# Optimization experiments

Hardware: AMD Instinct MI355X
Metric: run time of the kernel (lower is better)

Reference implementation:

```python
import jax, jax.numpy as jnp
import numpy as np

LR = 0.1
N_HEADS = 4


def setup_inputs() -> dict:
    key = jax.random.key(0)
    ks = jax.random.split(key, 12)
    B, S, D, M, H = 2, 1024, 128, 512, 512
    s = 0.05
    return {
        "x": jax.random.normal(ks[0], (B, S, D), jnp.float32),
        "memory": jax.random.normal(ks[1], (M, D), jnp.float32) * s,
        "w_q": jax.random.normal(ks[2], (D, D), jnp.float32) * s,
        "w_k": jax.random.normal(ks[3], (D, D), jnp.float32) * s,
        "w_v": jax.random.normal(ks[4], (D, D), jnp.float32) * s,
        "b_q": jax.random.normal(ks[5], (D,), jnp.float32) * s,
        "b_k": jax.random.normal(ks[6], (D,), jnp.float32) * s,
        "b_v": jax.random.normal(ks[7], (D,), jnp.float32) * s,
        "w_o": jax.random.normal(ks[8], (D, D), jnp.float32) * s,
        "b_o": jax.random.normal(ks[9], (D,), jnp.float32) * s,
        "w_fc": jax.random.normal(ks[10], (H, D), jnp.float32) * s,
        "b_fc": jax.random.normal(ks[11], (H,), jnp.float32) * s,
    }


def reference(x, memory, w_q, w_k, w_v, b_q, b_k, b_v, w_o, b_o, w_fc, b_fc):
    B, S, D = x.shape
    M = memory.shape[0]
    hd = D // N_HEADS

    # --- LongTermMemory update (broadcast pairwise diff [B,S,M,D]) ---
    diff = x[:, :, None, :] - memory[None, None, :, :]          # [B,S,M,D]
    surprise = jnp.sqrt(jnp.sum(diff * diff, axis=-1, keepdims=True))  # [B,S,M,1]
    agg = jnp.mean(LR * surprise * diff, axis=(0, 1))           # [M,D]
    # torch does memory.data += agg (detached in-place update)
    mem = memory + jax.lax.stop_gradient(agg)                    # [M,D]

    # --- MultiheadAttention(query=x, key=mem, value=mem), batch_first ---
    # mem is identical across batch, so project once.
    q = (x @ w_q.T + b_q).reshape(B, S, N_HEADS, hd)
    k = (mem @ w_k.T + b_k).reshape(M, N_HEADS, hd)
    v = (mem @ w_v.T + b_v).reshape(M, N_HEADS, hd)
    scores = jnp.einsum('bshd,mhd->bhsm', q, k) / jnp.sqrt(jnp.asarray(hd, x.dtype))
    attn = jax.nn.softmax(scores, axis=-1)
    ctx = jnp.einsum('bhsm,mhd->bshd', attn, v).reshape(B, S, D)
    attn_out = ctx @ w_o.T + b_o                                 # [B,S,D]

    # --- Linear + ReLU ---
    return jax.nn.relu(attn_out @ w_fc.T + b_fc)                 # [B,S,hidden]
```

## Files before the change

kernel.cpp:

```cpp
#include <hip/hip_runtime.h>
#include <hip/hip_bf16.h>
#include <math.h>

#define SS 1024
#define MM 512
#define LRC (0.1f/2048.0f)
#define SCALE 0.17677669529663687f

typedef __attribute__((ext_vector_type(8))) short s8v;
typedef __attribute__((ext_vector_type(4))) float f32x4;
#define MFMA16(a, b, c) __builtin_amdgcn_mfma_f32_16x16x32_bf16(a, b, c, 0, 0, 0)

__device__ __forceinline__ unsigned short f2b(float f) {
  union { float f; unsigned int u; } v; v.f = f;
  return (unsigned short)((v.u + 0x7FFFu + ((v.u >> 16) & 1u)) >> 16);
}

__global__ __launch_bounds__(256) void k_p1(
    const float* __restrict__ x, const float* __restrict__ mem,
    const float* __restrict__ wq, const float* __restrict__ wk,
    const float* __restrict__ wv, const float* __restrict__ wo,
    const float* __restrict__ wfc, const float* __restrict__ bq,
    unsigned short* __restrict__ STb, unsigned short* __restrict__ xT,
    unsigned short* __restrict__ qbf,
    unsigned short* __restrict__ wkb, unsigned short* __restrict__ wvb,
    unsigned short* __restrict__ wob, unsigned short* __restrict__ wfcb) {
  __shared__ alignas(16) char smem[69376];
  const int t = threadIdx.x, bx = blockIdx.x;
  const int w = t >> 6, l = t & 63;
  const int kq = (l >> 4) * 8;
  const int r0l = (l >> 4) * 4;

  if (bx < 256) {
    float (*xl)[132]          = reinterpret_cast<float (*)[132]>(smem);
    unsigned short (*xb)[136] = reinterpret_cast<unsigned short (*)[136]>(smem + 33792);
    unsigned short (*mb)[136] = reinterpret_cast<unsigned short (*)[136]>(smem + 51200);
    float* xn                 = reinterpret_cast<float*>(smem + 68608);
    float* mn                 = reinterpret_cast<float*>(smem + 68864);
    const int bs0 = (bx & 31) * 64, m0 = (bx >> 5) * 64;

    for (int i = t; i < 2048; i += 256) {
      int r = i >> 5, c4 = (i & 31) * 4;
      float4 v = *reinterpret_cast<const float4*>(&x[(bs0 + r) * 128 + c4]);
      xl[r][c4] = v.x; xl[r][c4+1] = v.y; xl[r][c4+2] = v.z; xl[r][c4+3] = v.w;
      ushort4 u; u.x = f2b(v.x); u.y = f2b(v.y); u.z = f2b(v.z); u.w = f2b(v.w);
      *reinterpret_cast<ushort4*>(&xb[r][c4]) = u;
    }
    __syncthreads();
    {
      int r = t >> 2, q = t & 3;
      float s = 0.f;
      #pragma unroll
      for (int j = 0; j < 32; ++j) { float v = xl[r][q * 32 + j]; s += v * v; }
      s += __shfl_xor(s, 1); s += __shfl_xor(s, 2);
      if (q == 0) xn[r] = s;
    }
    if ((bx >> 5) == 0) {
      int d = t >> 1, hh = t & 1;
      #pragma unroll
      for (int j4 = 0; j4 < 32; j4 += 4) {
        ushort4 u;
        u.x = xb[hh*32 + j4    ][d];
        u.y = xb[hh*32 + j4 + 1][d];
        u.z = xb[hh*32 + j4 + 2][d];
        u.w = xb[hh*32 + j4 + 3][d];
        *reinterpret_cast<ushort4*>(&xT[d * 2048 + bs0 + hh*32 + j4]) = u;
      }
    }
    __syncthreads();
    for (int i = t; i < 2048; i += 256) {
      int r = i >> 5, c4 = (i & 31) * 4;
      float4 v = *reinterpret_cast<const float4*>(&mem[(m0 + r) * 128 + c4]);
      xl[r][c4] = v.x; xl[r][c4+1] = v.y; xl[r][c4+2] = v.z; xl[r][c4+3] = v.w;
      ushort4 u; u.x = f2b(v.x); u.y = f2b(v.y); u.z = f2b(v.z); u.w = f2b(v.w);
      *reinterpret_cast<ushort4*>(&mb[r][c4]) = u;
    }
    __syncthreads();
    {
      int r = t >> 2, q = t & 3;
      float s = 0.f;
      #pragma unroll
      for (int j = 0; j < 32; ++j) { float v = xl[r][q * 32 + j]; s += v * v; }
      s += __shfl_xor(s, 1); s += __shfl_xor(s, 2);
      if (q == 0) mn[r] = s;
    }
    __syncthreads();
    f32x4 acc[4] = {};
    #pragma unroll
    for (int kc = 0; kc < 4; ++kc) {
      s8v a = *reinterpret_cast<const s8v*>(&xb[w*16 + (l&15)][kc*32 + kq]);
      #pragma unroll
      for (int mt = 0; mt < 4; ++mt) {
        s8v b = *reinterpret_cast<const s8v*>(&mb[mt*16 + (l&15)][kc*32 + kq]);
        acc[mt] = MFMA16(a, b, acc[mt]);
      }
    }
    const int r0g = bs0 + w * 16 + r0l;
    float xnr[4];
    #pragma unroll
    for (int i = 0; i < 4; ++i) xnr[i] = xn[w*16 + r0l + i];
    #pragma unroll
    for (int mt = 0; mt < 4; ++mt) {
      const int coll = mt * 16 + (l & 15);
      const float mnv = mn[coll];
      ushort4 u;
      u.x = f2b(sqrtf(fmaxf(0.f, xnr[0] + mnv - 2.f * acc[mt][0])));
      u.y = f2b(sqrtf(fmaxf(0.f, xnr[1] + mnv - 2.f * acc[mt][1])));
      u.z = f2b(sqrtf(fmaxf(0.f, xnr[2] + mnv - 2.f * acc[mt][2])));
      u.w = f2b(sqrtf(fmaxf(0.f, xnr[3] + mnv - 2.f * acc[mt][3])));
      *reinterpret_cast<ushort4*>(&STb[(m0 + coll) * 2048 + r0g]) = u;
    }
  } else if (bx < 288) {
    unsigned short (*xb)[136]  = reinterpret_cast<unsigned short (*)[136]>(smem);
    unsigned short (*wql)[136] = reinterpret_cast<unsigned short (*)[136]>(smem + 17408);
    const int s0 = (bx - 256) * 64;
    for (int i = t; i < 2048; i += 256) {
      int r = i >> 5, c4 = (i & 31) * 4;
      float4 v = *reinterpret_cast<const float4*>(&x[(s0 + r) * 128 + c4]);
      ushort4 u; u.x = f2b(v.x); u.y = f2b(v.y); u.z = f2b(v.z); u.w = f2b(v.w);
      *reinterpret_cast<ushort4*>(&xb[r][c4]) = u;
    }
    for (int i = t; i < 4096; i += 256) {
      int r = i >> 5, c4 = (i & 31) * 4;
      float4 v = *reinterpret_cast<const float4*>(&wq[r * 128 + c4]);
      ushort4 u; u.x = f2b(v.x); u.y = f2b(v.y); u.z = f2b(v.z); u.w = f2b(v.w);
      *reinterpret_cast<ushort4*>(&wql[r][c4]) = u;
    }
    __syncthreads();
    f32x4 acc[8] = {};
    #pragma unroll
    for (int kc = 0; kc < 4; ++kc) {
      s8v a = *reinterpret_cast<const s8v*>(&xb[w*16 + (l&15)][kc*32 + kq]);
      #pragma unroll
      for (int nt = 0; nt < 8; ++nt) {
        s8v b = *reinterpret_cast<const s8v*>(&wql[nt*16 + (l&15)][kc*32 + kq]);
        acc[nt] = MFMA16(a, b, acc[nt]);
      }
    }
    const int r0g = s0 + w * 16 + r0l;
    #pragma unroll
    for (int nt = 0; nt < 8; ++nt) {
      const int col = nt * 16 + (l & 15);
      const float bb = bq[col];
      #pragma unroll
      for (int i = 0; i < 4; ++i)
        qbf[(r0g + i) * 128 + col] = f2b((acc[nt][i] + bb) * SCALE);
    }
  } else {
    const float* src; unsigned short* dst; int off = 0;
    if (bx == 288)      { src = wk;  dst = wkb; }
    else if (bx == 289) { src = wv;  dst = wvb; }
    else if (bx == 290) { src = wo;  dst = wob; }
    else                { src = wfc; dst = wfcb; off = (bx - 291) * 16384; }
    for (int i = t; i < 4096; i += 256) {
      float4 v = *reinterpret_cast<const float4*>(&src[off + i * 4]);
      ushort4 u; u.x = f2b(v.x); u.y = f2b(v.y); u.z = f2b(v.z); u.w = f2b(v.w);
      *reinterpret_cast<ushort4*>(&dst[off + i * 4]) = u;
    }
  }
}

__global__ __launch_bounds__(256) void k_p2(
    const unsigned short* __restrict__ STb, const unsigned short* __restrict__ xT,
    const float* __restrict__ mem,
    const unsigned short* __restrict__ wkb, const unsigned short* __restrict__ wvb,
    const float* __restrict__ bk, const float* __restrict__ bv,
    unsigned short* __restrict__ kbf, unsigned short* __restrict__ vT) {
  __shared__ float Tld[16][132];
  __shared__ float srowl[16];
  __shared__ unsigned short mnl[16][136];
  const int t = threadIdx.x;
  const int w = t >> 6, l = t & 63;
  const int kq = (l >> 4) * 8;
  const int r0l = (l >> 4) * 4;
  const int m0 = blockIdx.x * 16;

  f32x4 acc[2] = {};
  float ssum = 0.f;
  const int arow = m0 + (l & 15);
  #pragma unroll 4
  for (int kk = 0; kk < 64; ++kk) {
    s8v a = *reinterpret_cast<const s8v*>(&STb[arow * 2048 + kk * 32 + kq]);
    #pragma unroll
    for (int j = 0; j < 8; ++j) {
      union { unsigned int u; float f; } cv;
      cv.u = ((unsigned int)(unsigned short)a[j]) << 16;
      ssum += cv.f;
    }
    #pragma unroll
    for (int nt = 0; nt < 2; ++nt) {
      s8v b = *reinterpret_cast<const s8v*>(&xT[(w*32 + nt*16 + (l&15)) * 2048 + kk*32 + kq]);
      acc[nt] = MFMA16(a, b, acc[nt]);
    }
  }
  ssum += __shfl_xor(ssum, 16); ssum += __shfl_xor(ssum, 32);
  if (w == 0 && l < 16) srowl[l] = ssum;
  #pragma unroll
  for (int nt = 0; nt < 2; ++nt) {
    const int col = w * 32 + nt * 16 + (l & 15);
    #pragma unroll
    for (int i = 0; i < 4; ++i) Tld[r0l + i][col] = acc[nt][i];
  }
  __syncthreads();
  #pragma unroll
  for (int i = 0; i < 8; ++i) {
    const int flat = t + 256 * i;
    const int r = flat >> 7, c = flat & 127;
    const float mv = mem[(m0 + r) * 128 + c];
    mnl[r][c] = f2b(mv + LRC * (Tld[r][c] - srowl[r] * mv));
  }
  __syncthreads();
  #pragma unroll
  for (int p = 0; p < 2; ++p) {
    const unsigned short* W = p ? wvb : wkb;
    const float* bias = p ? bv : bk;
    f32x4 pacc[2] = {};
    #pragma unroll
    for (int kc = 0; kc < 4; ++kc) {
      s8v a = *reinterpret_cast<const s8v*>(&mnl[l & 15][kc * 32 + kq]);
      #pragma unroll
      for (int nt = 0; nt < 2; ++nt) {
        s8v b = *reinterpret_cast<const s8v*>(&W[(w*32 + nt*16 + (l&15)) * 128 + kc*32 + kq]);
        pacc[nt] = MFMA16(a, b, pacc[nt]);
      }
    }
    #pragma unroll
    for (int nt = 0; nt < 2; ++nt) {
      const int col = w * 32 + nt * 16 + (l & 15);
      const float bb = bias[col];
      if (p == 0) {
        #pragma unroll
        for (int i = 0; i < 4; ++i)
          kbf[(m0 + r0l + i) * 128 + col] = f2b(pacc[nt][i] + bb);
      } else {
        ushort4 u;
        u.x = f2b(pacc[nt][0] + bb); u.y = f2b(pacc[nt][1] + bb);
        u.z = f2b(pacc[nt][2] + bb); u.w = f2b(pacc[nt][3] + bb);
        *reinterpret_cast<ushort4*>(&vT[col * 512 + m0 + r0l]) = u;
      }
    }
  }
}

__global__ __launch_bounds__(256) void k_p3(
    const unsigned short* __restrict__ qbf, const unsigned short* __restrict__ kbf,
    const unsigned short* __restrict__ vT, const unsigned short* __restrict__ wob,
    const unsigned short* __restrict__ wfcb, const float* __restrict__ bo,
    const float* __restrict__ bfc, float* __restrict__ out) {
  __shared__ alignas(16) char smem[75264];
  unsigned short (*Pl)[520] = reinterpret_cast<unsigned short (*)[520]>(smem);
  unsigned short (*cl)[136] = reinterpret_cast<unsigned short (*)[136]>(smem + 66560);
  unsigned short (*al)[136] = reinterpret_cast<unsigned short (*)[136]>(smem + 70912);
  const int t = threadIdx.x;
  const int w = t >> 6, l = t & 63;
  const int kq = (l >> 4) * 8;
  const int r0l = (l >> 4) * 4;
  const int r0 = blockIdx.x * 16;

  {
    const int h = w;
    const s8v a = *reinterpret_cast<const s8v*>(&qbf[(r0 + (l & 15)) * 128 + h * 32 + kq]);
    f32x4 acc[32];
    #pragma unroll
    for (int mt = 0; mt < 32; ++mt) acc[mt] = f32x4{0.f, 0.f, 0.f, 0.f};
    #pragma unroll
    for (int mt = 0; mt < 32; ++mt) {
      s8v b2 = *reinterpret_cast<const s8v*>(&kbf[(mt*16 + (l&15)) * 128 + h*32 + kq]);
      acc[mt] = MFMA16(a, b2, acc[mt]);
    }
    #pragma unroll
    for (int i = 0; i < 4; ++i) {
      float mx = acc[0][i];
      #pragma unroll
      for (int mt = 1; mt < 32; ++mt) mx = fmaxf(mx, acc[mt][i]);
      mx = fmaxf(mx, __shfl_xor(mx, 1));
      mx = fmaxf(mx, __shfl_xor(mx, 2));
      mx = fmaxf(mx, __shfl_xor(mx, 4));
      mx = fmaxf(mx, __shfl_xor(mx, 8));
      float sm = 0.f;
      #pragma unroll
      for (int mt = 0; mt < 32; ++mt) {
        float e = __expf(acc[mt][i] - mx); acc[mt][i] = e; sm += e;
      }
      sm += __shfl_xor(sm, 1); sm += __shfl_xor(sm, 2);
      sm += __shfl_xor(sm, 4); sm += __shfl_xor(sm, 8);
      const float inv = 1.f / sm;
      #pragma unroll
      for (int mt = 0; mt < 32; ++mt)
        Pl[h * 16 + r0l + i][mt * 16 + (l & 15)] = f2b(acc[mt][i] * inv);
    }
  }
  __syncthreads();
  {
    const int h = w;
    f32x4 acc[2] = {};
    #pragma unroll 4
    for (int kk = 0; kk < 16; ++kk) {
      s8v a = *reinterpret_cast<const s8v*>(&Pl[h * 16 + (l & 15)][kk * 32 + kq]);
      #pragma unroll
      for (int nt = 0; nt < 2; ++nt) {
        s8v b2 = *reinterpret_cast<const s8v*>(&vT[(h*32 + nt*16 + (l&15)) * 512 + kk*32 + kq]);
        acc[nt] = MFMA16(a, b2, acc[nt]);
      }
    }
    #pragma unroll
    for (int nt = 0; nt < 2; ++nt) {
      const int col = h * 32 + nt * 16 + (l & 15);
      #pragma unroll
      for (int i = 0; i < 4; ++i) cl[r0l + i][col] = f2b(acc[nt][i]);
    }
  }
  __syncthreads();
  {
    f32x4 acc[2] = {};
    #pragma unroll
    for (int kc = 0; kc < 4; ++kc) {
      s8v a = *reinterpret_cast<const s8v*>(&cl[l & 15][kc * 32 + kq]);
      #pragma unroll
      for (int nt = 0; nt < 2; ++nt) {
        s8v b2 = *reinterpret_cast<const s8v*>(&wob[(w*32 + nt*16 + (l&15)) * 128 + kc*32 + kq]);
        acc[nt] = MFMA16(a, b2, acc[nt]);
      }
    }
    #pragma unroll
    for (int nt = 0; nt < 2; ++nt) {
      const int col = w * 32 + nt * 16 + (l & 15);
      const float bb = bo[col];
      #pragma unroll
      for (int i = 0; i < 4; ++i) al[r0l + i][col] = f2b(acc[nt][i] + bb);
    }
  }
  __syncthreads();
  {
    f32x4 acc[8] = {};
    #pragma unroll
    for (int kc = 0; kc < 4; ++kc) {
      s8v a = *reinterpret_cast<const s8v*>(&al[l & 15][kc * 32 + kq]);
      #pragma unroll
      for (int nt = 0; nt < 8; ++nt) {
        s8v b2 = *reinterpret_cast<const s8v*>(&wfcb[(w*128 + nt*16 + (l&15)) * 128 + kc*32 + kq]);
        acc[nt] = MFMA16(a, b2, acc[nt]);
      }
    }
    #pragma unroll
    for (int nt = 0; nt < 8; ++nt) {
      const int col = w * 128 + nt * 16 + (l & 15);
      const float bb = bfc[col];
      #pragma unroll
      for (int i = 0; i < 4; ++i)
        out[(r0 + r0l + i) * 512 + col] = fmaxf(acc[nt][i] + bb, 0.f);
    }
  }
}

extern "C" void kernel_launch(void* const* d_in, const int* in_sizes, int n_in,
                              void* d_out, int out_size, void* d_ws, size_t ws_size,
                              hipStream_t stream) {
  const float* x    = (const float*)d_in[0];
  const float* mem  = (const float*)d_in[1];
  const float* w_q  = (const float*)d_in[2];
  const float* w_k  = (const float*)d_in[3];
  const float* w_v  = (const float*)d_in[4];
  const float* b_q  = (const float*)d_in[5];
  const float* b_k  = (const float*)d_in[6];
  const float* b_v  = (const float*)d_in[7];
  const float* w_o  = (const float*)d_in[8];
  const float* b_o  = (const float*)d_in[9];
  const float* w_fc = (const float*)d_in[10];
  const float* b_fc = (const float*)d_in[11];
  float* out = (float*)d_out;

  char* base = (char*)d_ws;
  unsigned short* STb  = (unsigned short*)(base);
  unsigned short* xT   = (unsigned short*)(base + 2097152);
  unsigned short* qbf  = (unsigned short*)(base + 2621440);
  unsigned short* kbf  = (unsigned short*)(base + 3145728);
  unsigned short* vT   = (unsigned short*)(base + 3276800);
  unsigned short* wkb  = (unsigned short*)(base + 3407872);
  unsigned short* wvb  = (unsigned short*)(base + 3440640);
  unsigned short* wob  = (unsigned short*)(base + 3473408);
  unsigned short* wfcb = (unsigned short*)(base + 3506176);

  k_p1<<<295, 256, 0, stream>>>(x, mem, w_q, w_k, w_v, w_o, w_fc, b_q,
                                STb, xT, qbf, wkb, wvb, wob, wfcb);
  k_p2<<<32, 256, 0, stream>>>(STb, xT, mem, wkb, wvb, b_k, b_v, kbf, vT);
  k_p3<<<128, 256, 0, stream>>>(qbf, kbf, vT, wob, wfcb, b_o, b_fc, out);
}
```

Measured before the change: 58.91 us.

## Move Q projection and weight casts into second kernel, slim first kernel

The first kernel now handles only the pairwise-distance tiles. It computes row norms from registers with wave shuffles instead of staging fp32 data in LDS, which lowers shared-memory use and removes barriers. The Q projection and the wo/wfc casts move into the second kernel, running alongside its 32 memory-update blocks so that the mostly idle second launch gets more parallel work. The memory-update blocks now cast wk/wv to bf16 themselves into LDS, so each of the 32 blocks repeats that conversion.

```diff
diff --git a/kernel.cpp b/kernel.cpp
--- a/kernel.cpp
+++ b/kernel.cpp
@@ -18,226 +18,258 @@
 
 __global__ __launch_bounds__(256) void k_p1(
     const float* __restrict__ x, const float* __restrict__ mem,
-    const float* __restrict__ wq, const float* __restrict__ wk,
-    const float* __restrict__ wv, const float* __restrict__ wo,
-    const float* __restrict__ wfc, const float* __restrict__ bq,
-    unsigned short* __restrict__ STb, unsigned short* __restrict__ xT,
-    unsigned short* __restrict__ qbf,
-    unsigned short* __restrict__ wkb, unsigned short* __restrict__ wvb,
-    unsigned short* __restrict__ wob, unsigned short* __restrict__ wfcb) {
-  __shared__ alignas(16) char smem[69376];
+    unsigned short* __restrict__ STb, unsigned short* __restrict__ xT) {
+  __shared__ unsigned short xb[64][136];
+  __shared__ unsigned short mb[64][136];
+  __shared__ float xn[64];
+  __shared__ float mn[64];
   const int t = threadIdx.x, bx = blockIdx.x;
   const int w = t >> 6, l = t & 63;
   const int kq = (l >> 4) * 8;
   const int r0l = (l >> 4) * 4;
-
-  if (bx < 256) {
-    float (*xl)[132]          = reinterpret_cast<float (*)[132]>(smem);
-    unsigned short (*xb)[136] = reinterpret_cast<unsigned short (*)[136]>(smem + 33792);
-    unsigned short (*mb)[136] = reinterpret_cast<unsigned short (*)[136]>(smem + 51200);
-    float* xn                 = reinterpret_cast<float*>(smem + 68608);
-    float* mn                 = reinterpret_cast<float*>(smem + 68864);
-    const int bs0 = (bx & 31) * 64, m0 = (bx >> 5) * 64;
-
-    for (int i = t; i < 2048; i += 256) {
-      int r = i >> 5, c4 = (i & 31) * 4;
-      float4 v = *reinterpret_cast<const float4*>(&x[(bs0 + r) * 128 + c4]);
-      xl[r][c4] = v.x; xl[r][c4+1] = v.y; xl[r][c4+2] = v.z; xl[r][c4+3] = v.w;
+  const int bs0 = (bx & 31) * 64, m0 = (bx >> 5) * 64;
+  const int rB = t >> 5;
+  const int c4 = (t & 31) * 4;
+
+  {
+    float p[8];
+    #pragma unroll
+    for (int k = 0; k < 8; ++k) {
+      const int r = rB + 8 * k;
+      const float4 v = *reinterpret_cast<const float4*>(&x[(bs0 + r) * 128 + c4]);
+      p[k] = v.x*v.x + v.y*v.y + v.z*v.z + v.w*v.w;
       ushort4 u; u.x = f2b(v.x); u.y = f2b(v.y); u.z = f2b(v.z); u.w = f2b(v.w);
       *reinterpret_cast<ushort4*>(&xb[r][c4]) = u;
     }
-    __syncthreads();
-    {
-      int r = t >> 2, q = t & 3;
-      float s = 0.f;
-      #pragma unroll
-      for (int j = 0; j < 32; ++j) { float v = xl[r][q * 32 + j]; s += v * v; }
-      s += __shfl_xor(s, 1); s += __shfl_xor(s, 2);
-      if (q == 0) xn[r] = s;
-    }
-    if ((bx >> 5) == 0) {
-      int d = t >> 1, hh = t & 1;
-      #pragma unroll
-      for (int j4 = 0; j4 < 32; j4 += 4) {
-        ushort4 u;
-        u.x = xb[hh*32 + j4    ][d];
-        u.y = xb[hh*32 + j4 + 1][d];
-        u.z = xb[hh*32 + j4 + 2][d];
-        u.w = xb[hh*32 + j4 + 3][d];
-        *reinterpret_cast<ushort4*>(&xT[d * 2048 + bs0 + hh*32 + j4]) = u;
-      }
-    }
-    __syncthreads();
-    for (int i = t; i < 2048; i += 256) {
-      int r = i >> 5, c4 = (i & 31) * 4;
-      float4 v = *reinterpret_cast<const float4*>(&mem[(m0 + r) * 128 + c4]);
-      xl[r][c4] = v.x; xl[r][c4+1] = v.y; xl[r][c4+2] = v.z; xl[r][c4+3] = v.w;
+    #pragma unroll
+    for (int k = 0; k < 8; ++k) {
+      float s = p[k];
+      s += __shfl_xor(s, 1);  s += __shfl_xor(s, 2);
+      s += __shfl_xor(s, 4);  s += __shfl_xor(s, 8);
+      s += __shfl_xor(s, 16);
+      if ((t & 31) == 0) xn[rB + 8 * k] = s;
+    }
+  }
+  {
+    float p[8];
+    #pragma unroll
+    for (int k = 0; k < 8; ++k) {
+      const int r = rB + 8 * k;
+      const float4 v = *reinterpret_cast<const float4*>(&mem[(m0 + r) * 128 + c4]);
+      p[k] = v.x*v.x + v.y*v.y + v.z*v.z + v.w*v.w;
       ushort4 u; u.x = f2b(v.x); u.y = f2b(v.y); u.z = f2b(v.z); u.w = f2b(v.w);
       *reinterpret_cast<ushort4*>(&mb[r][c4]) = u;
     }
-    __syncthreads();
-    {
-      int r = t >> 2, q = t & 3;
-      float s = 0.f;
-      #pragma unroll
-      for (int j = 0; j < 32; ++j) { float v = xl[r][q * 32 + j]; s += v * v; }
-      s += __shfl_xor(s, 1); s += __shfl_xor(s, 2);
-      if (q == 0) mn[r] = s;
-    }
-    __syncthreads();
-    f32x4 acc[4] = {};
-    #pragma unroll
-    for (int kc = 0; kc < 4; ++kc) {
-      s8v a = *reinterpret_cast<const s8v*>(&xb[w*16 + (l&15)][kc*32 + kq]);
-      #pragma unroll
-      for (int mt = 0; mt < 4; ++mt) {
-        s8v b = *reinterpret_cast<const s8v*>(&mb[mt*16 + (l&15)][kc*32 + kq]);
-        acc[mt] = MFMA16(a, b, acc[mt]);
-      }
-    }
-    const int r0g = bs0 + w * 16 + r0l;
-    float xnr[4];
-    #pragma unroll
-    for (int i = 0; i < 4; ++i) xnr[i] = xn[w*16 + r0l + i];
+    #pragma unroll
+    for (int k = 0; k < 8; ++k) {
+      float s = p[k];
+      s += __shfl_xor(s, 1);  s += __shfl_xor(s, 2);
+      s += __shfl_xor(s, 4);  s += __shfl_xor(s, 8);
+      s += __shfl_xor(s, 16);
+      if ((t & 31) == 0) mn[rB + 8 * k] = s;
+    }
+  }
+  __syncthreads();
+
+  if ((bx >> 5) == 0) {
+    int d = t >> 1, hh = t & 1;
+    #pragma unroll
+    for (int j4 = 0; j4 < 32; j4 += 4) {
+      ushort4 u;
+      u.x = xb[hh*32 + j4    ][d];
+      u.y = xb[hh*32 + j4 + 1][d];
+      u.z = xb[hh*32 + j4 + 2][d];
+      u.w = xb[hh*32 + j4 + 3][d];
+      *reinterpret_cast<ushort4*>(&xT[d * 2048 + bs0 + hh*32 + j4]) = u;
+    }
+  }
+
+  f32x4 acc[4] = {};
+  #pragma unroll
+  for (int kc = 0; kc < 4; ++kc) {
+    s8v a = *reinterpret_cast<const s8v*>(&xb[w*16 + (l&15)][kc*32 + kq]);
     #pragma unroll
     for (int mt = 0; mt < 4; ++mt) {
-      const int coll = mt * 16 + (l & 15);
-      const float mnv = mn[coll];
-      ushort4 u;
-      u.x = f2b(sqrtf(fmaxf(0.f, xnr[0] + mnv - 2.f * acc[mt][0])));
-      u.y = f2b(sqrtf(fmaxf(0.f, xnr[1] + mnv - 2.f * acc[mt][1])));
-      u.z = f2b(sqrtf(fmaxf(0.f, xnr[2] + mnv - 2.f * acc[mt][2])));
-      u.w = f2b(sqrtf(fmaxf(0.f, xnr[3] + mnv - 2.f * acc[mt][3])));
-      *reinterpret_cast<ushort4*>(&STb[(m0 + coll) * 2048 + r0g]) = u;
-    }
-  } else if (bx < 288) {
-    unsigned short (*xb)[136]  = reinterpret_cast<unsigned short (*)[136]>(smem);
-    unsigned short (*wql)[136] = reinterpret_cast<unsigned short (*)[136]>(smem + 17408);
-    const int s0 = (bx - 256) * 64;
-    for (int i = t; i < 2048; i += 256) {
-      int r = i >> 5, c4 = (i & 31) * 4;
-      float4 v = *reinterpret_cast<const float4*>(&x[(s0 + r) * 128 + c4]);
-      ushort4 u; u.x = f2b(v.x); u.y = f2b(v.y); u.z = f2b(v.z); u.w = f2b(v.w);
-      *reinterpret_cast<ushort4*>(&xb[r][c4]) = u;
-    }
-    for (int i = t; i < 4096; i += 256) {
-      int r = i >> 5, c4 = (i & 31) * 4;
-      float4 v = *reinterpret_cast<const float4*>(&wq[r * 128 + c4]);
-      ushort4 u; u.x = f2b(v.x); u.y = f2b(v.y); u.z = f2b(v.z); u.w = f2b(v.w);
-      *reinterpret_cast<ushort4*>(&wql[r][c4]) = u;
-    }
-    __syncthreads();
-    f32x4 acc[8] = {};
-    #pragma unroll
-    for (int kc = 0; kc < 4; ++kc) {
-      s8v a = *reinterpret_cast<const s8v*>(&xb[w*16 + (l&15)][kc*32 + kq]);
-      #pragma unroll
-      for (int nt = 0; nt < 8; ++nt) {
-        s8v b = *reinterpret_cast<const s8v*>(&wql[nt*16 + (l&15)][kc*32 + kq]);
-        acc[nt] = MFMA16(a, b, acc[nt]);
-      }
-    }
-    const int r0g = s0 + w * 16 + r0l;
-    #pragma unroll
-    for (int nt = 0; nt < 8; ++nt) {
-      const int col = nt * 16 + (l & 15);
-      const float bb = bq[col];
-      #pragma unroll
-      for (int i = 0; i < 4; ++i)
-        qbf[(r0g + i) * 128 + col] = f2b((acc[nt][i] + bb) * SCALE);
-    }
-  } else {
-    const float* src; unsigned short* dst; int off = 0;
-    if (bx == 288)      { src = wk;  dst = wkb; }
-    else if (bx == 289) { src = wv;  dst = wvb; }
-    else if (bx == 290) { src = wo;  dst = wob; }
-    else                { src = wfc; dst = wfcb; off = (bx - 291) * 16384; }
-    for (int i = t; i < 4096; i += 256) {
-      float4 v = *reinterpret_cast<const float4*>(&src[off + i * 4]);
-      ushort4 u; u.x = f2b(v.x); u.y = f2b(v.y); u.z = f2b(v.z); u.w = f2b(v.w);
-      *reinterpret_cast<ushort4*>(&dst[off + i * 4]) = u;
-    }
+      s8v b = *reinterpret_cast<const s8v*>(&mb[mt*16 + (l&15)][kc*32 + kq]);
+      acc[mt] = MFMA16(a, b, acc[mt]);
+    }
+  }
+  const int r0g = bs0 + w * 16 + r0l;
+  float xnr[4];
+  #pragma unroll
+  for (int i = 0; i < 4; ++i) xnr[i] = xn[w*16 + r0l + i];
+  #pragma unroll
+  for (int mt = 0; mt < 4; ++mt) {
+    const int coll = mt * 16 + (l & 15);
+    const float mnv = mn[coll];
+    ushort4 u;
+    u.x = f2b(sqrtf(fmaxf(0.f, xnr[0] + mnv - 2.f * acc[mt][0])));
+    u.y = f2b(sqrtf(fmaxf(0.f, xnr[1] + mnv - 2.f * acc[mt][1])));
+    u.z = f2b(sqrtf(fmaxf(0.f, xnr[2] + mnv - 2.f * acc[mt][2])));
+    u.w = f2b(sqrtf(fmaxf(0.f, xnr[3] + mnv - 2.f * acc[mt][3])));
+    *reinterpret_cast<ushort4*>(&STb[(m0 + coll) * 2048 + r0g]) = u;
   }
 }
 
 __global__ __launch_bounds__(256) void k_p2(
     const unsigned short* __restrict__ STb, const unsigned short* __restrict__ xT,
-    const float* __restrict__ mem,
-    const unsigned short* __restrict__ wkb, const unsigned short* __restrict__ wvb,
-    const float* __restrict__ bk, const float* __restrict__ bv,
-    unsigned short* __restrict__ kbf, unsigned short* __restrict__ vT) {
-  __shared__ float Tld[16][132];
-  __shared__ float srowl[16];
-  __shared__ unsigned short mnl[16][136];
-  const int t = threadIdx.x;
+    const float* __restrict__ x, const float* __restrict__ mem,
+    const float* __restrict__ wq, const float* __restrict__ wk,
+    const float* __restrict__ wv, const float* __restrict__ wo,
+    const float* __restrict__ wfc,
+    const float* __restrict__ bq, const float* __restrict__ bk,
+    const float* __restrict__ bv,
+    unsigned short* __restrict__ qbf, unsigned short* __restrict__ kbf,
+    unsigned short* __restrict__ vT,
+    unsigned short* __restrict__ wob, unsigned short* __restrict__ wfcb) {
+  __shared__ alignas(16) char smem[52224];
+  const int t = threadIdx.x, bx = blockIdx.x;
   const int w = t >> 6, l = t & 63;
   const int kq = (l >> 4) * 8;
   const int r0l = (l >> 4) * 4;
-  const int m0 = blockIdx.x * 16;
-
-  f32x4 acc[2] = {};
-  float ssum = 0.f;
-  const int arow = m0 + (l & 15);
-  #pragma unroll 4
-  for (int kk = 0; kk < 64; ++kk) {
-    s8v a = *reinterpret_cast<const s8v*>(&STb[arow * 2048 + kk * 32 + kq]);
-    #pragma unroll
-    for (int j = 0; j < 8; ++j) {
-      union { unsigned int u; float f; } cv;
-      cv.u = ((unsigned int)(unsigned short)a[j]) << 16;
-      ssum += cv.f;
-    }
-    #pragma unroll
-    for (int nt = 0; nt < 2; ++nt) {
-      s8v b = *reinterpret_cast<const s8v*>(&xT[(w*32 + nt*16 + (l&15)) * 2048 + kk*32 + kq]);
-      acc[nt] = MFMA16(a, b, acc[nt]);
-    }
-  }
-  ssum += __shfl_xor(ssum, 16); ssum += __shfl_xor(ssum, 32);
-  if (w == 0 && l < 16) srowl[l] = ssum;
-  #pragma unroll
-  for (int nt = 0; nt < 2; ++nt) {
-    const int col = w * 32 + nt * 16 + (l & 15);
-    #pragma unroll
-    for (int i = 0; i < 4; ++i) Tld[r0l + i][col] = acc[nt][i];
-  }
-  __syncthreads();
-  #pragma unroll
-  for (int i = 0; i < 8; ++i) {
-    const int flat = t + 256 * i;
-    const int r = flat >> 7, c = flat & 127;
-    const float mv = mem[(m0 + r) * 128 + c];
-    mnl[r][c] = f2b(mv + LRC * (Tld[r][c] - srowl[r] * mv));
-  }
-  __syncthreads();
-  #pragma unroll
-  for (int p = 0; p < 2; ++p) {
-    const unsigned short* W = p ? wvb : wkb;
-    const float* bias = p ? bv : bk;
-    f32x4 pacc[2] = {};
-    #pragma unroll
-    for (int kc = 0; kc < 4; ++kc) {
-      s8v a = *reinterpret_cast<const s8v*>(&mnl[l & 15][kc * 32 + kq]);
+
+  if (bx < 32) {
+    float (*Tld)[132]          = reinterpret_cast<float (*)[132]>(smem);
+    float* srowl               = reinterpret_cast<float*>(smem + 8448);
+    unsigned short (*mnl)[136] = reinterpret_cast<unsigned short (*)[136]>(smem + 8512);
+    unsigned short (*wl)[136]  = reinterpret_cast<unsigned short (*)[136]>(smem + 12864);
+    const int m0 = bx * 16;
+
+    f32x4 acc[2] = {};
+    float ssum = 0.f;
+    const int arow = m0 + (l & 15);
+    #pragma unroll 4
+    for (int kk = 0; kk < 64; ++kk) {
+      s8v a = *reinterpret_cast<const s8v*>(&STb[arow * 2048 + kk * 32 + kq]);
+      #pragma unroll
+      for (int j = 0; j < 8; ++j) {
+        union { unsigned int u; float f; } cv;
+        cv.u = ((unsigned int)(unsigned short)a[j]) << 16;
+        ssum += cv.f;
+      }
       #pragma unroll
       for (int nt = 0; nt < 2; ++nt) {
-        s8v b = *reinterpret_cast<const s8v*>(&W[(w*32 + nt*16 + (l&15)) * 128 + kc*32 + kq]);
-        pacc[nt] = MFMA16(a, b, pacc[nt]);
-      }
-    }
+        s8v b = *reinterpret_cast<const s8v*>(&xT[(w*32 + nt*16 + (l&15)) * 2048 + kk*32 + kq]);
+        acc[nt] = MFMA16(a, b, acc[nt]);
+      }
+    }
+    ssum += __shfl_xor(ssum, 16); ssum += __shfl_xor(ssum, 32);
+    if (w == 0 && l < 16) srowl[l] = ssum;
     #pragma unroll
     for (int nt = 0; nt < 2; ++nt) {
       const int col = w * 32 + nt * 16 + (l & 15);
-      const float bb = bias[col];
-      if (p == 0) {
+      #pragma unroll
+      for (int i = 0; i < 4; ++i) Tld[r0l + i][col] = acc[nt][i];
+    }
+    __syncthreads();
+    #pragma unroll
+    for (int i = 0; i < 8; ++i) {
+      const int flat = t + 256 * i;
+      const int r = flat >> 7, c = flat & 127;
+      const float mv = mem[(m0 + r) * 128 + c];
+      mnl[r][c] = f2b(mv + LRC * (Tld[r][c] - srowl[r] * mv));
+    }
+    __syncthreads();
+    for (int i = t; i < 4096; i += 256) {
+      int r = i >> 5, c4 = (i & 31) * 4;
+      float4 v = *reinterpret_cast<const float4*>(&wk[r * 128 + c4]);
+      ushort4 u; u.x = f2b(v.x); u.y = f2b(v.y); u.z = f2b(v.z); u.w = f2b(v.w);
+      *reinterpret_cast<ushort4*>(&wl[r][c4]) = u;
+    }
+    __syncthreads();
+    {
+      f32x4 pacc[2] = {};
+      #pragma unroll
+      for (int kc = 0; kc < 4; ++kc) {
+        s8v a = *reinterpret_cast<const s8v*>(&mnl[l & 15][kc * 32 + kq]);
+        #pragma unroll
+        for (int nt = 0; nt < 2; ++nt) {
+          s8v b = *reinterpret_cast<const s8v*>(&wl[(w*32 + nt*16 + (l&15))][kc*32 + kq]);
+          pacc[nt] = MFMA16(a, b, pacc[nt]);
+        }
+      }
+      #pragma unroll
+      for (int nt = 0; nt < 2; ++nt) {
+        const int col = w * 32 + nt * 16 + (l & 15);
+        const float bb = bk[col];
         #pragma unroll
         for (int i = 0; i < 4; ++i)
           kbf[(m0 + r0l + i) * 128 + col] = f2b(pacc[nt][i] + bb);
-      } else {
+      }
+    }
+    __syncthreads();
+    for (int i = t; i < 4096; i += 256) {
+      int r = i >> 5, c4 = (i & 31) * 4;
+      float4 v = *reinterpret_cast<const float4*>(&wv[r * 128 + c4]);
+      ushort4 u; u.x = f2b(v.x); u.y = f2b(v.y); u.z = f2b(v.z); u.w = f2b(v.w);
+      *reinterpret_cast<ushort4*>(&wl[r][c4]) = u;
+    }
+    __syncthreads();
+    {
+      f32x4 pacc[2] = {};
+      #pragma unroll
+      for (int kc = 0; kc < 4; ++kc) {
+        s8v a = *reinterpret_cast<const s8v*>(&mnl[l & 15][kc * 32 + kq]);
+        #pragma unroll
+        for (int nt = 0; nt < 2; ++nt) {
+          s8v b = *reinterpret_cast<const s8v*>(&wl[(w*32 + nt*16 + (l&15))][kc*32 + kq]);
+          pacc[nt] = MFMA16(a, b, pacc[nt]);
+        }
+      }
+      #pragma unroll
+      for (int nt = 0; nt < 2; ++nt) {
+        const int col = w * 32 + nt * 16 + (l & 15);
+        const float bb = bv[col];
         ushort4 u;
         u.x = f2b(pacc[nt][0] + bb); u.y = f2b(pacc[nt][1] + bb);
         u.z = f2b(pacc[nt][2] + bb); u.w = f2b(pacc[nt][3] + bb);
         *reinterpret_cast<ushort4*>(&vT[col * 512 + m0 + r0l]) = u;
       }
+    }
+  } else if (bx < 64) {
+    unsigned short (*xb)[136]  = reinterpret_cast<unsigned short (*)[136]>(smem);
+    unsigned short (*wql)[136] = reinterpret_cast<unsigned short (*)[136]>(smem + 17408);
+    const int s0 = (bx - 32) * 64;
+    for (int i = t; i < 2048; i += 256) {
+      int r = i >> 5, c4 = (i & 31) * 4;
+      float4 v = *reinterpret_cast<const float4*>(&x[(s0 + r) * 128 + c4]);
+      ushort4 u; u.x = f2b(v.x); u.y = f2b(v.y); u.z = f2b(v.z); u.w = f2b(v.w);
+      *reinterpret_cast<ushort4*>(&xb[r][c4]) = u;
+    }
+    for (int i = t; i < 4096; i += 256) {
+      int r = i >> 5, c4 = (i & 31) * 4;
+      float4 v = *reinterpret_cast<const float4*>(&wq[r * 128 + c4]);
+      ushort4 u; u.x = f2b(v.x); u.y = f2b(v.y); u.z = f2b(v.z); u.w = f2b(v.w);
+      *reinterpret_cast<ushort4*>(&wql[r][c4]) = u;
+    }
+    __syncthreads();
+    f32x4 acc[8] = {};
+    #pragma unroll
+    for (int kc = 0; kc < 4; ++kc) {
+      s8v a = *reinterpret_cast<const s8v*>(&xb[w*16 + (l&15)][kc*32 + kq]);
+      #pragma unroll
+      for (int nt = 0; nt < 8; ++nt) {
+        s8v b = *reinterpret_cast<const s8v*>(&wql[nt*16 + (l&15)][kc*32 + kq]);
+        acc[nt] = MFMA16(a, b, acc[nt]);
+      }
+    }
+    const int r0g = s0 + w * 16 + r0l;
+    #pragma unroll
+    for (int nt = 0; nt < 8; ++nt) {
+      const int col = nt * 16 + (l & 15);
+      const float bb = bq[col];
+      #pragma unroll
+      for (int i = 0; i < 4; ++i)
+        qbf[(r0g + i) * 128 + col] = f2b((acc[nt][i] + bb) * SCALE);
+    }
+  } else {
+    const float* src; unsigned short* dst; int off = 0;
+    if (bx == 64) { src = wo;  dst = wob; }
+    else          { src = wfc; dst = wfcb; off = (bx - 65) * 16384; }
+    for (int i = t; i < 4096; i += 256) {
+      float4 v = *reinterpret_cast<const float4*>(&src[off + i * 4]);
+      ushort4 u; u.x = f2b(v.x); u.y = f2b(v.y); u.z = f2b(v.z); u.w = f2b(v.w);
+      *reinterpret_cast<ushort4*>(&dst[off + i * 4]) = u;
     }
   }
 }
@@ -376,13 +408,11 @@
   unsigned short* qbf  = (unsigned short*)(base + 2621440);
   unsigned short* kbf  = (unsigned short*)(base + 3145728);
   unsigned short* vT   = (unsigned short*)(base + 3276800);
-  unsigned short* wkb  = (unsigned short*)(base + 3407872);
-  unsigned short* wvb  = (unsigned short*)(base + 3440640);
-  unsigned short* wob  = (unsigned short*)(base + 3473408);
-  unsigned short* wfcb = (unsigned short*)(base + 3506176);
-
-  k_p1<<<295, 256, 0, stream>>>(x, mem, w_q, w_k, w_v, w_o, w_fc, b_q,
-                                STb, xT, qbf, wkb, wvb, wob, wfcb);
-  k_p2<<<32, 256, 0, stream>>>(STb, xT, mem, wkb, wvb, b_k, b_v, kbf, vT);
+  unsigned short* wob  = (unsigned short*)(base + 3407872);
+  unsigned short* wfcb = (unsigned short*)(base + 3440640);
+
+  k_p1<<<256, 256, 0, stream>>>(x, mem, STb, xT);
+  k_p2<<<69, 256, 0, stream>>>(STb, xT, x, mem, w_q, w_k, w_v, w_o, w_fc,
+                               b_q, b_k, b_v, qbf, kbf, vT, wob, wfcb);
   k_p3<<<128, 256, 0, stream>>>(qbf, kbf, vT, wob, wfcb, b_o, b_fc, out);
 }
```

New measurement: 60.68 us. +3.0%, slower.
